# Performance work log

Hardware: AMD Instinct MI355X
Metric: run time of the kernel (lower is better)

The kernel has to match this reference:

```python
import jax, jax.numpy as jnp
import numpy as np
import math

B, S, D, H, L = 16, 1024, 256, 8, 4
OBS, ACT = 160, 96
DH = D // H  # 32, even as required by RoPE
ROPE_BASE = 10000.0
LN_EPS = 1e-5


def setup_inputs() -> dict:
    key = jax.random.key(0)
    ks = jax.random.split(key, 16)
    s = 0.02
    n = jax.random.normal
    return {
        "obs_seq": n(ks[0], (B, S, OBS), jnp.float32),
        "action_seq": n(ks[1], (B, S, ACT), jnp.float32),
        # linears stored as [in, out] (transpose of torch convention)
        "in_W": n(ks[2], (OBS + ACT, D), jnp.float32) * s,
        "in_b": jnp.zeros((D,), jnp.float32),
        "qW": n(ks[3], (L, D, D), jnp.float32) * s,
        "qb": jnp.zeros((L, D), jnp.float32),
        "kW": n(ks[4], (L, D, D), jnp.float32) * s,
        "kb": jnp.zeros((L, D), jnp.float32),
        "vW": n(ks[5], (L, D, D), jnp.float32) * s,
        "vb": jnp.zeros((L, D), jnp.float32),
        "oW": n(ks[6], (L, D, D), jnp.float32) * s,
        "ob": jnp.zeros((L, D), jnp.float32),
        "out_W": n(ks[7], (D, D), jnp.float32) * s,
        "out_b": jnp.zeros((D,), jnp.float32),
        "ln_g": jnp.ones((D,), jnp.float32),
        "ln_b": jnp.zeros((D,), jnp.float32),
    }


def _rope(x):
    # x: [B,H,S,DH]; interleaved real/imag rotation (stride-2 split like torch code)
    pos = jnp.arange(S, dtype=jnp.float32)[:, None]                 # [S,1]
    freq_seq = jnp.arange(0, DH, 2, dtype=jnp.float32)              # [DH/2]
    inv_freq = 1.0 / (ROPE_BASE ** (freq_seq / DH))
    freqs = pos * inv_freq[None, :]                                  # [S,DH/2]
    cos = jnp.cos(freqs)[None, None]                                 # [1,1,S,DH/2]
    sin = jnp.sin(freqs)[None, None]
    xr = x[..., 0::2]
    xi = x[..., 1::2]
    rr = xr * cos - xi * sin
    ri = xr * sin + xi * cos
    # interleave back: [..., DH/2, 2] -> [..., DH]
    return jnp.stack([rr, ri], axis=-1).reshape(x.shape)


def _attn_layer(x, qW, qb, kW, kb, vW, vb, oW, ob):
    def heads(t):
        return t.reshape(B, S, H, DH).transpose(0, 2, 1, 3)  # [B,H,S,DH]
    q = _rope(heads(x @ qW + qb))
    k = _rope(heads(x @ kW + kb))
    v = heads(x @ vW + vb)
    scores = jnp.einsum('bhqd,bhkd->bhqk', q, k) / math.sqrt(DH)
    w = jax.nn.softmax(scores, axis=-1)  # dropout is identity at inference
    o = jnp.einsum('bhqk,bhkd->bhqd', w, v)
    o = o.transpose(0, 2, 1, 3).reshape(B, S, D)
    return o @ oW + ob


def reference(obs_seq, action_seq, in_W, in_b, qW, qb, kW, kb, vW, vb, oW, ob,
              out_W, out_b, ln_g, ln_b):
    x = jnp.concatenate([obs_seq, action_seq], axis=-1) @ in_W + in_b  # [B,S,D]
    for l in range(L):  # residual self-attention stack with RoPE
        x = x + _attn_layer(x, qW[l], qb[l], kW[l], kb[l], vW[l], vb[l], oW[l], ob[l])
    y = x @ out_W + out_b
    mu = jnp.mean(y, axis=-1, keepdims=True)
    var = jnp.mean(jnp.square(y - mu), axis=-1, keepdims=True)
    y = (y - mu) / jnp.sqrt(var + LN_EPS) * ln_g + ln_b
    context_embedding = y[:, -1]       # seq_lengths=None path: last timestep
    sequence_embeddings = y
    return context_embedding, sequence_embeddings
```

## Files before the change

kernel.cpp:

```cpp
#include <hip/hip_runtime.h>
#include <hip/hip_bf16.h>
#include <math.h>

#define B_ 16
#define S_ 1024
#define D_ 256
#define H_ 8
#define L_ 4
#define DH_ 32
#define OBS_ 160
#define ACT_ 96
#define M_ (B_*S_)

typedef __attribute__((ext_vector_type(8)))  short short8v;
typedef __attribute__((ext_vector_type(4)))  short short4v;
typedef __attribute__((ext_vector_type(4)))  float f32x4;
typedef __attribute__((ext_vector_type(4)))  unsigned uint4v;

#define ALPHA_ 0.25507313f

__device__ inline short bf16rne(float x) {
    unsigned u = __builtin_bit_cast(unsigned, x);
    unsigned r = (u + 0x7fffu + ((u >> 16) & 1u)) >> 16;
    return (short)r;
}

#if __has_builtin(__builtin_amdgcn_exp2f)
#define EXP2F(x) __builtin_amdgcn_exp2f(x)
#else
#define EXP2F(x) exp2f(x)
#endif

__device__ inline unsigned cvtpk_bf16(float lo, float hi) {
    unsigned r;
    asm("v_cvt_pk_bf16_f32 %0, %1, %2" : "=v"(r) : "v"(lo), "v"(hi));
    return r;
}

__global__ __launch_bounds__(256) void rope_table_k(float* __restrict__ cosT2,
                                                    float* __restrict__ sinT2) {
    int idx = blockIdx.x * 256 + threadIdx.x;
    int i = idx >> 10, s = idx & 1023;
    float invf = powf(10000.0f, -(float)(2 * i) / 32.0f);
    float ang = (float)s * invf;
    float sn, cs;
    sincosf(ang, &sn, &cs);
    cosT2[idx] = cs;
    sinT2[idx] = sn;
}

__global__ __launch_bounds__(256) void cvt_in_k(const float* __restrict__ obs,
                                                const float* __restrict__ act,
                                                short* __restrict__ xIn) {
    const int idx = (blockIdx.x * 256 + threadIdx.x) * 8;
    const int row = idx >> 8, col = idx & 255;
    const float* s = (col < OBS_) ? (obs + (size_t)row * OBS_ + col)
                                  : (act + (size_t)row * ACT_ + (col - OBS_));
    const float4 v0 = *(const float4*)s;
    const float4 v1 = *(const float4*)(s + 4);
    short8v o = {bf16rne(v0.x), bf16rne(v0.y), bf16rne(v0.z), bf16rne(v0.w),
                 bf16rne(v1.x), bf16rne(v1.y), bf16rne(v1.z), bf16rne(v1.w)};
    *(short8v*)&xIn[idx] = o;
}

__global__ __launch_bounds__(256) void wconv_k(
    const float* __restrict__ qW, const float* __restrict__ kW,
    const float* __restrict__ vW, const float* __restrict__ oW,
    const float* __restrict__ outW, const float* __restrict__ inW,
    short* __restrict__ WTqkv, short* __restrict__ WTo,
    short* __restrict__ WTf, short* __restrict__ WTin)
{
    __shared__ float T[64][65];
    const int z = blockIdx.y;
    const int bx = blockIdx.x;
    const int tr = (bx & 3) * 64, tc = (bx >> 2) * 64;
    const float* src;
    short* dst;
    if (z < 16) {
        int lay = z >> 2, w = z & 3;
        if (w == 0)      { src = qW + lay * 65536; dst = WTqkv + lay * 196608; }
        else if (w == 1) { src = kW + lay * 65536; dst = WTqkv + lay * 196608 + 65536; }
        else if (w == 2) { src = vW + lay * 65536; dst = WTqkv + lay * 196608 + 131072; }
        else             { src = oW + lay * 65536; dst = WTo + lay * 65536; }
    } else if (z == 16) { src = outW; dst = WTf; }
    else                { src = inW;  dst = WTin; }
    const int tid = threadIdx.x;
    #pragma unroll
    for (int it = 0; it < 4; ++it) {
        int r = (tid >> 4) + it * 16, c = (tid & 15) * 4;
        *(float4*)&T[r][c] = *(const float4*)&src[(size_t)(tr + r) * 256 + tc + c];
    }
    __syncthreads();
    #pragma unroll
    for (int it = 0; it < 4; ++it) {
        int n = (tid >> 4) + it * 16, k = (tid & 15) * 4;
        short4v o = {bf16rne(T[k][n]), bf16rne(T[k + 1][n]),
                     bf16rne(T[k + 2][n]), bf16rne(T[k + 3][n])};
        *(short4v*)&dst[(size_t)(tc + n) * 256 + tr + k] = o;
    }
}

template<int EPI>
__global__ __launch_bounds__(256) void gemm_k(
    const short* __restrict__ A, const short* __restrict__ WT,
    const float* __restrict__ bq, const float* __restrict__ bk,
    const float* __restrict__ bv,
    float* __restrict__ xF, short* __restrict__ xB,
    short* __restrict__ Q2, short* __restrict__ K2, short* __restrict__ VT,
    float* __restrict__ yF,
    const float* __restrict__ cosT2, const float* __restrict__ sinT2)
{
    __shared__ short As[2][128 * 32];
    __shared__ short Bs[2][64 * 32];
    const int tid = threadIdx.x;
    const int l = tid & 63;
    const int wid = tid >> 6, wr = wid >> 1, wc = wid & 1;
    const int bn = blockIdx.x * 64, bm = blockIdx.y * 128;

    const short* aSrc0 = A + (size_t)(bm + (tid >> 2)) * 256 + (tid & 3) * 8;
    const short* aSrc1 = aSrc0 + 64 * 256;
    const short* bSrc  = WT + (size_t)(bn + (tid >> 2)) * 256 + (tid & 3) * 8;

    short8v a0 = *(const short8v*)aSrc0;
    short8v a1 = *(const short8v*)aSrc1;
    short8v b0 = *(const short8v*)bSrc;
    *(short8v*)&As[0][tid * 8]         = a0;
    *(short8v*)&As[0][(tid + 256) * 8] = a1;
    *(short8v*)&Bs[0][tid * 8]         = b0;
    __syncthreads();

    f32x4 acc[4][2];
    #pragma unroll
    for (int i = 0; i < 4; ++i)
        #pragma unroll
        for (int j = 0; j < 2; ++j) acc[i][j] = (f32x4){0.f, 0.f, 0.f, 0.f};

    #pragma unroll
    for (int t = 0; t < 8; ++t) {
        const int cur = t & 1;
        short8v na0, na1, nb;
        if (t < 7) {
            const int k = (t + 1) * 32;
            na0 = *(const short8v*)&aSrc0[k];
            na1 = *(const short8v*)&aSrc1[k];
            nb  = *(const short8v*)&bSrc[k];
        }
        short8v af[4], bf[2];
        #pragma unroll
        for (int i = 0; i < 4; ++i)
            af[i] = *(const short8v*)&As[cur][(wr * 64 + i * 16 + (l & 15)) * 32 + (l >> 4) * 8];
        #pragma unroll
        for (int j = 0; j < 2; ++j)
            bf[j] = *(const short8v*)&Bs[cur][(wc * 32 + j * 16 + (l & 15)) * 32 + (l >> 4) * 8];
        #pragma unroll
        for (int i = 0; i < 4; ++i)
            #pragma unroll
            for (int j = 0; j < 2; ++j)
                acc[i][j] = __builtin_amdgcn_mfma_f32_16x16x32_bf16(af[i], bf[j], acc[i][j], 0, 0, 0);
        if (t < 7) {
            const int nxt = cur ^ 1;
            *(short8v*)&As[nxt][tid * 8]         = na0;
            *(short8v*)&As[nxt][(tid + 256) * 8] = na1;
            *(short8v*)&Bs[nxt][tid * 8]         = nb;
            __syncthreads();
        }
    }

    if (EPI == 0) {
        const int region = bn >> 8;
        if (region == 2) {
            #pragma unroll
            for (int i = 0; i < 4; ++i) {
                const int m0 = bm + wr * 64 + i * 16 + ((l >> 4) << 2);
                const int bI = m0 >> 10, s0 = m0 & 1023;
                const int w  = s0 & 31;
                const int sp = (s0 & ~31) | ((((w & 15) >> 2) << 3) | ((w >> 4) << 2));
                #pragma unroll
                for (int j = 0; j < 2; ++j) {
                    const int nl = (bn & 255) + wc * 32 + j * 16 + (l & 15);
                    const float bb = bv[nl];
                    const f32x4 v = acc[i][j];
                    const int h = nl >> 5, dhh = nl & 31;
                    short4v o = {bf16rne(v[0] + bb), bf16rne(v[1] + bb),
                                 bf16rne(v[2] + bb), bf16rne(v[3] + bb)};
                    *(short4v*)&VT[((size_t)((bI * 8 + h) * 32 + dhh) << 10) + sp] = o;
                }
            }
        } else {
            const float* bias = (region == 0) ? bq : bk;
            __syncthreads();
            short* scr = &As[0][0];
            #pragma unroll
            for (int i = 0; i < 4; ++i) {
                const int tl0 = wr * 64 + i * 16 + ((l >> 4) << 2);
                const int s0r = (bm + tl0) & 1023;
                #pragma unroll
                for (int j = 0; j < 2; ++j) {
                    const int ncl = wc * 32 + j * 16 + (l & 15);
                    const int nl = (bn & 255) + ncl;
                    const float bb = bias[nl];
                    f32x4 v = acc[i][j];
                    v[0] += bb; v[1] += bb; v[2] += bb; v[3] += bb;
                    if (region == 0) { v *= ALPHA_; }
                    const int ir = (nl & 31) >> 1;
                    const f32x4 cs = *(const f32x4*)&cosT2[ir * 1024 + s0r];
                    const f32x4 sn = *(const f32x4*)&sinT2[ir * 1024 + s0r];
                    f32x4 pr;
                    #pragma unroll
                    for (int c = 0; c < 4; ++c) pr[c] = __shfl_xor(v[c], 1);
                    const float sg = (nl & 1) ? 1.f : -1.f;
                    #pragma unroll
                    for (int c = 0; c < 4; ++c)
                        v[c] = v[c] * cs[c] + sg * pr[c] * sn[c];
                    #pragma unroll
                    for (int c = 0; c < 4; ++c) {
                        const int tl = tl0 + c;
                        const int pos = (((ncl >> 3) ^ (tl & 7)) << 3) | (ncl & 7);
                        scr[tl * 64 + pos] = bf16rne(v[c]);
                    }
                }
            }
            __syncthreads();
            const int r = tid >> 1, h2 = tid & 1;
            const int tok = bm + r;
            const int bI = tok >> 10, s0 = tok & 1023;
            const int hh = ((bn & 255) >> 5) + h2;
            short* dst = ((region == 0) ? Q2 : K2)
                         + ((size_t)((bI * 8 + hh) * 1024 + s0)) * 32;
            #pragma unroll
            for (int k = 0; k < 4; ++k) {
                const int pos = ((h2 * 4 + k) ^ (r & 7)) << 3;
                *(uint4*)&dst[k * 8] = *(const uint4*)&scr[r * 64 + pos];
            }
        }
    } else {
        #pragma unroll
        for (int i = 0; i < 4; ++i) {
            const int m0 = bm + wr * 64 + i * 16 + ((l >> 4) << 2);
            #pragma unroll
            for (int j = 0; j < 2; ++j) {
                const int nn = bn + wc * 32 + j * 16 + (l & 15);
                const float bb = bq[nn];
                const f32x4 v = acc[i][j];
                #pragma unroll
                for (int c = 0; c < 4; ++c) {
                    float rr = v[c] + bb;
                    const size_t off = (size_t)(m0 + c) * 256 + nn;
                    if (EPI == 1) rr += xF[off];
                    if (EPI == 3) {
                        yF[off] = rr;
                    } else {
                        xF[off] = rr;
                        xB[off] = bf16rne(rr);
                    }
                }
            }
        }
    }
}

__global__ __launch_bounds__(512, 8) void attn_k(
    const short* __restrict__ Q2, const short* __restrict__ K2,
    const short* __restrict__ VT, short* __restrict__ O)
{
    __shared__ short LB[4096];
    const int tid = threadIdx.x;
    const int l = tid & 63, wid = tid >> 6;
    const int head = blockIdx.x & 127;
    const int qt = blockIdx.x >> 7;
    const int q0w = qt * 128 + wid * 16;
    const int lq = l & 15, g = l >> 4;

    const short8v Qf = *(const short8v*)&Q2[((size_t)head * 1024 + q0w + lq) * 32 + g * 8];

    const char* rbase = (const char*)LB + lq * 64 + ((g ^ ((lq >> 1) & 3)) << 4);

    const bool stg = (tid < 256);
    const int  sK  = (tid < 128) ? 1 : 0;
    const int  srow = (tid & 127) >> 2;
    const int  sc   = tid & 3;
    const short* gsrc = nullptr;
    int gstep = 0;
    char* wbase = nullptr;
    if (stg) {
        if (sK) { gsrc = K2 + ((size_t)head * 1024 + srow) * 32 + sc * 8; gstep = 1024; }
        else    { gsrc = VT + ((size_t)head * 32 + srow) * 1024 + sc * 8; gstep = 32; }
        wbase = (char*)LB + (sK ? 0 : 2048) + srow * 64 + ((sc ^ ((srow >> 1) & 3)) << 4);
    }

    f32x4 acc0 = {0.f, 0.f, 0.f, 0.f}, acc1 = {0.f, 0.f, 0.f, 0.f};
    const f32x4 z4 = {0.f, 0.f, 0.f, 0.f};
    float lsum = 0.f;
    short8v r = {};

    if (stg) {
        short8v r0 = *(const short8v*)gsrc; gsrc += gstep;
        r          = *(const short8v*)gsrc; gsrc += gstep;
        *(short8v*)wbase = r0;
    }
    __syncthreads();

#define ATTN_STEP(BUFOFF) do {                                                 \
        short8v Kf0 = *(const short8v*)(rbase + (BUFOFF));                     \
        short8v Kf1 = *(const short8v*)(rbase + (BUFOFF) + 1024);              \
        short8v Vf0 = *(const short8v*)(rbase + (BUFOFF) + 2048);              \
        short8v Vf1 = *(const short8v*)(rbase + (BUFOFF) + 3072);              \
        f32x4 s0 = __builtin_amdgcn_mfma_f32_16x16x32_bf16(Kf0, Qf, z4, 0,0,0);\
        f32x4 s1 = __builtin_amdgcn_mfma_f32_16x16x32_bf16(Kf1, Qf, z4, 0,0,0);\
        float p0 = EXP2F(s0[0]), p1 = EXP2F(s0[1]);                            \
        float p2 = EXP2F(s0[2]), p3 = EXP2F(s0[3]);                            \
        float p4 = EXP2F(s1[0]), p5 = EXP2F(s1[1]);                            \
        float p6 = EXP2F(s1[2]), p7 = EXP2F(s1[3]);                            \
        lsum += ((p0 + p1) + (p2 + p3)) + ((p4 + p5) + (p6 + p7));             \
        uint4v pv = {cvtpk_bf16(p0, p1), cvtpk_bf16(p2, p3),                   \
                     cvtpk_bf16(p4, p5), cvtpk_bf16(p6, p7)};                  \
        short8v Pf = __builtin_bit_cast(short8v, pv);                          \
        acc0 = __builtin_amdgcn_mfma_f32_16x16x32_bf16(Vf0, Pf, acc0, 0,0,0);  \
        acc1 = __builtin_amdgcn_mfma_f32_16x16x32_bf16(Vf1, Pf, acc1, 0,0,0);  \
    } while (0)

    #pragma unroll 1
    for (int i = 0; i < 15; ++i) {
        if (stg) { *(short8v*)(wbase + 4096) = r;
                   r = *(const short8v*)gsrc; gsrc += gstep; }
        ATTN_STEP(0);
        __syncthreads();
        if (stg) { *(short8v*)wbase = r;
                   r = *(const short8v*)gsrc; gsrc += gstep; }
        ATTN_STEP(4096);
        __syncthreads();
    }
    if (stg) { *(short8v*)(wbase + 4096) = r; }
    ATTN_STEP(0);
    __syncthreads();
    ATTN_STEP(4096);
#undef ATTN_STEP

    lsum += __shfl_xor(lsum, 16);
    lsum += __shfl_xor(lsum, 32);
    const float inv = 1.f / lsum;
    const int bI = head >> 3, hh = head & 7;
    short* op = O + ((size_t)(bI * 1024 + q0w + lq)) * 256 + hh * 32 + g * 4;
    short4v o0 = {bf16rne(acc0[0] * inv), bf16rne(acc0[1] * inv),
                  bf16rne(acc0[2] * inv), bf16rne(acc0[3] * inv)};
    short4v o1 = {bf16rne(acc1[0] * inv), bf16rne(acc1[1] * inv),
                  bf16rne(acc1[2] * inv), bf16rne(acc1[3] * inv)};
    *(short4v*)op = o0;
    *(short4v*)(op + 16) = o1;
}

__global__ __launch_bounds__(256) void ln_k(
    const float* __restrict__ y, const float* __restrict__ g,
    const float* __restrict__ bta, float* __restrict__ outp)
{
    const int tid = threadIdx.x;
    const int wave = tid >> 6, lane = tid & 63;
    const int row = blockIdx.x * 4 + wave;
    const int col = lane * 4;
    float4 t = *(const float4*)&y[(size_t)row * 256 + col];
    float sum = t.x + t.y + t.z + t.w;
    float ss  = t.x * t.x + t.y * t.y + t.z * t.z + t.w * t.w;
    #pragma unroll
    for (int off = 32; off; off >>= 1) {
        sum += __shfl_xor(sum, off);
        ss  += __shfl_xor(ss, off);
    }
    float mean = sum * (1.f / 256.f);
    float var  = ss * (1.f / 256.f) - mean * mean;
    float rstd = rsqrtf(var + 1e-5f);
    float4 gv = *(const float4*)&g[col];
    float4 bv = *(const float4*)&bta[col];
    float4 o;
    o.x = (t.x - mean) * rstd * gv.x + bv.x;
    o.y = (t.y - mean) * rstd * gv.y + bv.y;
    o.z = (t.z - mean) * rstd * gv.z + bv.z;
    o.w = (t.w - mean) * rstd * gv.w + bv.w;
    float* seq = outp + B_ * D_;
    *(float4*)&seq[(size_t)row * 256 + col] = o;
    if ((row & (S_ - 1)) == S_ - 1)
        *(float4*)&outp[(size_t)(row >> 10) * 256 + col] = o;
}

extern "C" void kernel_launch(void* const* d_in, const int* in_sizes, int n_in,
                              void* d_out, int out_size, void* d_ws, size_t ws_size,
                              hipStream_t stream)
{
    const float* obs  = (const float*)d_in[0];
    const float* act  = (const float*)d_in[1];
    const float* inW  = (const float*)d_in[2];
    const float* inb  = (const float*)d_in[3];
    const float* qW   = (const float*)d_in[4];
    const float* qb   = (const float*)d_in[5];
    const float* kW   = (const float*)d_in[6];
    const float* kb   = (const float*)d_in[7];
    const float* vW   = (const float*)d_in[8];
    const float* vb   = (const float*)d_in[9];
    const float* oW   = (const float*)d_in[10];
    const float* ob   = (const float*)d_in[11];
    const float* outW = (const float*)d_in[12];
    const float* outb = (const float*)d_in[13];
    const float* lng  = (const float*)d_in[14];
    const float* lnb  = (const float*)d_in[15];
    float* outp = (float*)d_out;

    const size_t MD = (size_t)M_ * D_;
    float* xF    = (float*)d_ws;
    short* xB    = (short*)(xF + MD);
    short* xIn   = xB + MD;
    short* Q2    = xIn + MD;
    short* K2    = Q2 + MD;
    short* VT    = K2 + MD;
    short* Obf   = VT + MD;
    short* WTqkv = Obf + MD;
    short* WTo   = WTqkv + 786432;
    short* WTf   = WTo + 262144;
    short* WTin  = WTf + 65536;
    float* cosT2 = (float*)(WTin + 65536);
    float* sinT2 = cosT2 + 16384;
    float* ybuf  = (float*)Q2;

    rope_table_k<<<64, 256, 0, stream>>>(cosT2, sinT2);
    cvt_in_k<<<2048, 256, 0, stream>>>(obs, act, xIn);
    wconv_k<<<dim3(16, 18), 256, 0, stream>>>(qW, kW, vW, oW, outW, inW,
                                              WTqkv, WTo, WTf, WTin);

    gemm_k<2><<<dim3(4, 128), 256, 0, stream>>>(xIn, WTin, inb, nullptr, nullptr,
            xF, xB, nullptr, nullptr, nullptr, nullptr, nullptr, nullptr);

    for (int lay = 0; lay < L_; ++lay) {
        gemm_k<0><<<dim3(12, 128), 256, 0, stream>>>(xB, WTqkv + lay * 196608,
                qb + lay * 256, kb + lay * 256, vb + lay * 256,
                nullptr, nullptr, Q2, K2, VT, nullptr, cosT2, sinT2);
        attn_k<<<1024, 512, 0, stream>>>(Q2, K2, VT, Obf);
        gemm_k<1><<<dim3(4, 128), 256, 0, stream>>>(Obf, WTo + lay * 65536,
                ob + lay * 256, nullptr, nullptr, xF, xB,
                nullptr, nullptr, nullptr, nullptr, nullptr, nullptr);
    }

    gemm_k<3><<<dim3(4, 128), 256, 0, stream>>>(xB, WTf, outb, nullptr, nullptr,
            nullptr, nullptr, nullptr, nullptr, nullptr, ybuf, nullptr, nullptr);
    ln_k<<<M_ / 4, 256, 0, stream>>>(ybuf, lng, lnb, outp);
}
```

Baseline: 309.2 us.

## Process two 16-query tiles per wave in attention to reuse K/V loads

Each attention wave now handles 32 query rows (two 16-row Q fragments) instead of 16, so every K/V fragment read from shared memory and every staged K/V tile feeds twice as many MFMAs. The grid is halved to 512 blocks and the occupancy hint drops from 8 to 4 blocks per CU to allow for the extra registers. The aim is to cut LDS traffic, global K/V staging and barrier overhead per unit of work. The cost is higher register pressure and fewer blocks to spread across the CUs.

```diff
diff --git a/kernel.cpp b/kernel.cpp
--- a/kernel.cpp
+++ b/kernel.cpp
@@ -259,7 +259,7 @@
     }
 }
 
-__global__ __launch_bounds__(512, 8) void attn_k(
+__global__ __launch_bounds__(512, 4) void attn_k(
     const short* __restrict__ Q2, const short* __restrict__ K2,
     const short* __restrict__ VT, short* __restrict__ O)
 {
@@ -268,10 +268,12 @@
     const int l = tid & 63, wid = tid >> 6;
     const int head = blockIdx.x & 127;
     const int qt = blockIdx.x >> 7;
-    const int q0w = qt * 128 + wid * 16;
+    const int q0w = qt * 256 + wid * 32;
     const int lq = l & 15, g = l >> 4;
 
-    const short8v Qf = *(const short8v*)&Q2[((size_t)head * 1024 + q0w + lq) * 32 + g * 8];
+    const short* qp = &Q2[((size_t)head * 1024 + q0w + lq) * 32 + g * 8];
+    const short8v QfA = *(const short8v*)qp;
+    const short8v QfB = *(const short8v*)(qp + 16 * 32);
 
     const char* rbase = (const char*)LB + lq * 64 + ((g ^ ((lq >> 1) & 3)) << 4);
 
@@ -288,9 +290,10 @@
         wbase = (char*)LB + (sK ? 0 : 2048) + srow * 64 + ((sc ^ ((srow >> 1) & 3)) << 4);
     }
 
-    f32x4 acc0 = {0.f, 0.f, 0.f, 0.f}, acc1 = {0.f, 0.f, 0.f, 0.f};
+    f32x4 aA0 = {0.f,0.f,0.f,0.f}, aA1 = {0.f,0.f,0.f,0.f};
+    f32x4 aB0 = {0.f,0.f,0.f,0.f}, aB1 = {0.f,0.f,0.f,0.f};
     const f32x4 z4 = {0.f, 0.f, 0.f, 0.f};
-    float lsum = 0.f;
+    float lsA = 0.f, lsB = 0.f;
     short8v r = {};
 
     if (stg) {
@@ -305,18 +308,30 @@
         short8v Kf1 = *(const short8v*)(rbase + (BUFOFF) + 1024);              \
         short8v Vf0 = *(const short8v*)(rbase + (BUFOFF) + 2048);              \
         short8v Vf1 = *(const short8v*)(rbase + (BUFOFF) + 3072);              \
-        f32x4 s0 = __builtin_amdgcn_mfma_f32_16x16x32_bf16(Kf0, Qf, z4, 0,0,0);\
-        f32x4 s1 = __builtin_amdgcn_mfma_f32_16x16x32_bf16(Kf1, Qf, z4, 0,0,0);\
-        float p0 = EXP2F(s0[0]), p1 = EXP2F(s0[1]);                            \
-        float p2 = EXP2F(s0[2]), p3 = EXP2F(s0[3]);                            \
-        float p4 = EXP2F(s1[0]), p5 = EXP2F(s1[1]);                            \
-        float p6 = EXP2F(s1[2]), p7 = EXP2F(s1[3]);                            \
-        lsum += ((p0 + p1) + (p2 + p3)) + ((p4 + p5) + (p6 + p7));             \
-        uint4v pv = {cvtpk_bf16(p0, p1), cvtpk_bf16(p2, p3),                   \
-                     cvtpk_bf16(p4, p5), cvtpk_bf16(p6, p7)};                  \
-        short8v Pf = __builtin_bit_cast(short8v, pv);                          \
-        acc0 = __builtin_amdgcn_mfma_f32_16x16x32_bf16(Vf0, Pf, acc0, 0,0,0);  \
-        acc1 = __builtin_amdgcn_mfma_f32_16x16x32_bf16(Vf1, Pf, acc1, 0,0,0);  \
+        f32x4 sA0 = __builtin_amdgcn_mfma_f32_16x16x32_bf16(Kf0, QfA, z4, 0,0,0);\
+        f32x4 sA1 = __builtin_amdgcn_mfma_f32_16x16x32_bf16(Kf1, QfA, z4, 0,0,0);\
+        f32x4 sB0 = __builtin_amdgcn_mfma_f32_16x16x32_bf16(Kf0, QfB, z4, 0,0,0);\
+        f32x4 sB1 = __builtin_amdgcn_mfma_f32_16x16x32_bf16(Kf1, QfB, z4, 0,0,0);\
+        float pa0 = EXP2F(sA0[0]), pa1 = EXP2F(sA0[1]);                        \
+        float pa2 = EXP2F(sA0[2]), pa3 = EXP2F(sA0[3]);                        \
+        float pa4 = EXP2F(sA1[0]), pa5 = EXP2F(sA1[1]);                        \
+        float pa6 = EXP2F(sA1[2]), pa7 = EXP2F(sA1[3]);                        \
+        lsA += ((pa0 + pa1) + (pa2 + pa3)) + ((pa4 + pa5) + (pa6 + pa7));      \
+        uint4v pva = {cvtpk_bf16(pa0, pa1), cvtpk_bf16(pa2, pa3),              \
+                      cvtpk_bf16(pa4, pa5), cvtpk_bf16(pa6, pa7)};             \
+        short8v PfA = __builtin_bit_cast(short8v, pva);                        \
+        aA0 = __builtin_amdgcn_mfma_f32_16x16x32_bf16(Vf0, PfA, aA0, 0,0,0);   \
+        aA1 = __builtin_amdgcn_mfma_f32_16x16x32_bf16(Vf1, PfA, aA1, 0,0,0);   \
+        float pb0 = EXP2F(sB0[0]), pb1 = EXP2F(sB0[1]);                        \
+        float pb2 = EXP2F(sB0[2]), pb3 = EXP2F(sB0[3]);                        \
+        float pb4 = EXP2F(sB1[0]), pb5 = EXP2F(sB1[1]);                        \
+        float pb6 = EXP2F(sB1[2]), pb7 = EXP2F(sB1[3]);                        \
+        lsB += ((pb0 + pb1) + (pb2 + pb3)) + ((pb4 + pb5) + (pb6 + pb7));      \
+        uint4v pvb = {cvtpk_bf16(pb0, pb1), cvtpk_bf16(pb2, pb3),              \
+                      cvtpk_bf16(pb4, pb5), cvtpk_bf16(pb6, pb7)};             \
+        short8v PfB = __builtin_bit_cast(short8v, pvb);                        \
+        aB0 = __builtin_amdgcn_mfma_f32_16x16x32_bf16(Vf0, PfB, aB0, 0,0,0);   \
+        aB1 = __builtin_amdgcn_mfma_f32_16x16x32_bf16(Vf1, PfB, aB1, 0,0,0);   \
     } while (0)
 
     #pragma unroll 1
@@ -336,17 +351,27 @@
     ATTN_STEP(4096);
 #undef ATTN_STEP
 
-    lsum += __shfl_xor(lsum, 16);
-    lsum += __shfl_xor(lsum, 32);
-    const float inv = 1.f / lsum;
+    lsA += __shfl_xor(lsA, 16);
+    lsA += __shfl_xor(lsA, 32);
+    lsB += __shfl_xor(lsB, 16);
+    lsB += __shfl_xor(lsB, 32);
+    const float invA = 1.f / lsA;
+    const float invB = 1.f / lsB;
     const int bI = head >> 3, hh = head & 7;
     short* op = O + ((size_t)(bI * 1024 + q0w + lq)) * 256 + hh * 32 + g * 4;
-    short4v o0 = {bf16rne(acc0[0] * inv), bf16rne(acc0[1] * inv),
-                  bf16rne(acc0[2] * inv), bf16rne(acc0[3] * inv)};
-    short4v o1 = {bf16rne(acc1[0] * inv), bf16rne(acc1[1] * inv),
-                  bf16rne(acc1[2] * inv), bf16rne(acc1[3] * inv)};
-    *(short4v*)op = o0;
-    *(short4v*)(op + 16) = o1;
+    short4v oA0 = {bf16rne(aA0[0] * invA), bf16rne(aA0[1] * invA),
+                   bf16rne(aA0[2] * invA), bf16rne(aA0[3] * invA)};
+    short4v oA1 = {bf16rne(aA1[0] * invA), bf16rne(aA1[1] * invA),
+                   bf16rne(aA1[2] * invA), bf16rne(aA1[3] * invA)};
+    *(short4v*)op = oA0;
+    *(short4v*)(op + 16) = oA1;
+    short* opB = op + 16 * 256;
+    short4v oB0 = {bf16rne(aB0[0] * invB), bf16rne(aB0[1] * invB),
+                   bf16rne(aB0[2] * invB), bf16rne(aB0[3] * invB)};
+    short4v oB1 = {bf16rne(aB1[0] * invB), bf16rne(aB1[1] * invB),
+                   bf16rne(aB1[2] * invB), bf16rne(aB1[3] * invB)};
+    *(short4v*)opB = oB0;
+    *(short4v*)(opB + 16) = oB1;
 }
 
 __global__ __launch_bounds__(256) void ln_k(
@@ -431,7 +456,7 @@
         gemm_k<0><<<dim3(12, 128), 256, 0, stream>>>(xB, WTqkv + lay * 196608,
                 qb + lay * 256, kb + lay * 256, vb + lay * 256,
                 nullptr, nullptr, Q2, K2, VT, nullptr, cosT2, sinT2);
-        attn_k<<<1024, 512, 0, stream>>>(Q2, K2, VT, Obf);
+        attn_k<<<512, 512, 0, stream>>>(Q2, K2, VT, Obf);
         gemm_k<1><<<dim3(4, 128), 256, 0, stream>>>(Obf, WTo + lay * 65536,
                 ob + lay * 256, nullptr, nullptr, xF, xB,
                 nullptr, nullptr, nullptr, nullptr, nullptr, nullptr);
```

Measured after the change: 308.4 us. No clear change (-0.2%).

## Stage whole per-head K/V in LDS and process 64 queries per wave

Applied to the files above, without the earlier changes.

The attention kernel now copies the full K and V for one head (128 KB) into shared memory once. It then loops over all keys with no barriers, and each wave handles four 16-query fragments that reuse every K/V fragment read from shared memory. The grid drops from 1024 to 256 blocks and the launch bound allows only two blocks per CU. This removes the double-buffered per-step staging and its per-step __syncthreads. In exchange, occupancy falls to roughly one block per CU, and the up-front global-to-LDS load can no longer overlap with compute.

```diff
diff --git a/kernel.cpp b/kernel.cpp
--- a/kernel.cpp
+++ b/kernel.cpp
@@ -259,94 +259,99 @@
     }
 }
 
-__global__ __launch_bounds__(512, 8) void attn_k(
+__global__ __launch_bounds__(512, 2) void attn_k(
     const short* __restrict__ Q2, const short* __restrict__ K2,
     const short* __restrict__ VT, short* __restrict__ O)
 {
-    __shared__ short LB[4096];
+    __shared__ short lb[65536];
     const int tid = threadIdx.x;
     const int l = tid & 63, wid = tid >> 6;
     const int head = blockIdx.x & 127;
-    const int qt = blockIdx.x >> 7;
-    const int q0w = qt * 128 + wid * 16;
+    const int qh = blockIdx.x >> 7;
+    const int q0w = qh * 512 + wid * 64;
     const int lq = l & 15, g = l >> 4;
 
-    const short8v Qf = *(const short8v*)&Q2[((size_t)head * 1024 + q0w + lq) * 32 + g * 8];
-
-    const char* rbase = (const char*)LB + lq * 64 + ((g ^ ((lq >> 1) & 3)) << 4);
-
-    const bool stg = (tid < 256);
-    const int  sK  = (tid < 128) ? 1 : 0;
-    const int  srow = (tid & 127) >> 2;
-    const int  sc   = tid & 3;
-    const short* gsrc = nullptr;
-    int gstep = 0;
-    char* wbase = nullptr;
-    if (stg) {
-        if (sK) { gsrc = K2 + ((size_t)head * 1024 + srow) * 32 + sc * 8; gstep = 1024; }
-        else    { gsrc = VT + ((size_t)head * 32 + srow) * 1024 + sc * 8; gstep = 32; }
-        wbase = (char*)LB + (sK ? 0 : 2048) + srow * 64 + ((sc ^ ((srow >> 1) & 3)) << 4);
-    }
-
-    f32x4 acc0 = {0.f, 0.f, 0.f, 0.f}, acc1 = {0.f, 0.f, 0.f, 0.f};
+    const short* Kh = K2 + (size_t)head * 32768;
+    const short* Vh = VT + (size_t)head * 32768;
+
+    #pragma unroll
+    for (int i = 0; i < 8; ++i) {
+        const int c = tid + i * 512;
+        short8v kv = *(const short8v*)(Kh + c * 8);
+        const int key = c >> 2, dc = c & 3;
+        *(short8v*)((char*)lb + key * 64 + ((dc ^ ((key >> 1) & 3)) << 4)) = kv;
+        short8v vv = *(const short8v*)(Vh + c * 8);
+        const int dh = c >> 7, kc = c & 127;
+        *(short8v*)((char*)lb + 65536 + (kc >> 2) * 2048 + dh * 64
+                    + (((kc & 3) ^ ((dh >> 1) & 3)) << 4)) = vv;
+    }
+
+    const short* qp = Q2 + ((size_t)head * 1024 + q0w + lq) * 32 + g * 8;
+    const short8v QfA = *(const short8v*)qp;
+    const short8v QfB = *(const short8v*)(qp + 512);
+    const short8v QfC = *(const short8v*)(qp + 1024);
+    const short8v QfD = *(const short8v*)(qp + 1536);
+
+    const char* LBK = (const char*)lb + lq * 64 + ((g ^ ((lq >> 1) & 3)) << 4);
+    const char* LBV = LBK + 65536;
+
+    f32x4 aA0 = {0.f,0.f,0.f,0.f}, aA1 = {0.f,0.f,0.f,0.f};
+    f32x4 aB0 = {0.f,0.f,0.f,0.f}, aB1 = {0.f,0.f,0.f,0.f};
+    f32x4 aC0 = {0.f,0.f,0.f,0.f}, aC1 = {0.f,0.f,0.f,0.f};
+    f32x4 aD0 = {0.f,0.f,0.f,0.f}, aD1 = {0.f,0.f,0.f,0.f};
     const f32x4 z4 = {0.f, 0.f, 0.f, 0.f};
-    float lsum = 0.f;
-    short8v r = {};
-
-    if (stg) {
-        short8v r0 = *(const short8v*)gsrc; gsrc += gstep;
-        r          = *(const short8v*)gsrc; gsrc += gstep;
-        *(short8v*)wbase = r0;
-    }
+    float lsA = 0.f, lsB = 0.f, lsC = 0.f, lsD = 0.f;
+
     __syncthreads();
 
-#define ATTN_STEP(BUFOFF) do {                                                 \
-        short8v Kf0 = *(const short8v*)(rbase + (BUFOFF));                     \
-        short8v Kf1 = *(const short8v*)(rbase + (BUFOFF) + 1024);              \
-        short8v Vf0 = *(const short8v*)(rbase + (BUFOFF) + 2048);              \
-        short8v Vf1 = *(const short8v*)(rbase + (BUFOFF) + 3072);              \
-        f32x4 s0 = __builtin_amdgcn_mfma_f32_16x16x32_bf16(Kf0, Qf, z4, 0,0,0);\
-        f32x4 s1 = __builtin_amdgcn_mfma_f32_16x16x32_bf16(Kf1, Qf, z4, 0,0,0);\
+#define QSTEP(QF, A0, A1, LS) do {                                             \
+        f32x4 s0 = __builtin_amdgcn_mfma_f32_16x16x32_bf16(Kf0, QF, z4, 0,0,0);\
+        f32x4 s1 = __builtin_amdgcn_mfma_f32_16x16x32_bf16(Kf1, QF, z4, 0,0,0);\
         float p0 = EXP2F(s0[0]), p1 = EXP2F(s0[1]);                            \
         float p2 = EXP2F(s0[2]), p3 = EXP2F(s0[3]);                            \
         float p4 = EXP2F(s1[0]), p5 = EXP2F(s1[1]);                            \
         float p6 = EXP2F(s1[2]), p7 = EXP2F(s1[3]);                            \
-        lsum += ((p0 + p1) + (p2 + p3)) + ((p4 + p5) + (p6 + p7));             \
+        LS += ((p0 + p1) + (p2 + p3)) + ((p4 + p5) + (p6 + p7));               \
         uint4v pv = {cvtpk_bf16(p0, p1), cvtpk_bf16(p2, p3),                   \
                      cvtpk_bf16(p4, p5), cvtpk_bf16(p6, p7)};                  \
         short8v Pf = __builtin_bit_cast(short8v, pv);                          \
-        acc0 = __builtin_amdgcn_mfma_f32_16x16x32_bf16(Vf0, Pf, acc0, 0,0,0);  \
-        acc1 = __builtin_amdgcn_mfma_f32_16x16x32_bf16(Vf1, Pf, acc1, 0,0,0);  \
+        A0 = __builtin_amdgcn_mfma_f32_16x16x32_bf16(Vf0, Pf, A0, 0,0,0);      \
+        A1 = __builtin_amdgcn_mfma_f32_16x16x32_bf16(Vf1, Pf, A1, 0,0,0);      \
     } while (0)
 
-    #pragma unroll 1
-    for (int i = 0; i < 15; ++i) {
-        if (stg) { *(short8v*)(wbase + 4096) = r;
-                   r = *(const short8v*)gsrc; gsrc += gstep; }
-        ATTN_STEP(0);
-        __syncthreads();
-        if (stg) { *(short8v*)wbase = r;
-                   r = *(const short8v*)gsrc; gsrc += gstep; }
-        ATTN_STEP(4096);
-        __syncthreads();
-    }
-    if (stg) { *(short8v*)(wbase + 4096) = r; }
-    ATTN_STEP(0);
-    __syncthreads();
-    ATTN_STEP(4096);
-#undef ATTN_STEP
-
-    lsum += __shfl_xor(lsum, 16);
-    lsum += __shfl_xor(lsum, 32);
-    const float inv = 1.f / lsum;
+    #pragma unroll 4
+    for (int t = 0; t < 32; ++t) {
+        const short8v Kf0 = *(const short8v*)(LBK + t * 2048);
+        const short8v Kf1 = *(const short8v*)(LBK + t * 2048 + 1024);
+        const short8v Vf0 = *(const short8v*)(LBV + t * 2048);
+        const short8v Vf1 = *(const short8v*)(LBV + t * 2048 + 1024);
+        QSTEP(QfA, aA0, aA1, lsA);
+        QSTEP(QfB, aB0, aB1, lsB);
+        QSTEP(QfC, aC0, aC1, lsC);
+        QSTEP(QfD, aD0, aD1, lsD);
+    }
+#undef QSTEP
+
+    lsA += __shfl_xor(lsA, 16); lsA += __shfl_xor(lsA, 32);
+    lsB += __shfl_xor(lsB, 16); lsB += __shfl_xor(lsB, 32);
+    lsC += __shfl_xor(lsC, 16); lsC += __shfl_xor(lsC, 32);
+    lsD += __shfl_xor(lsD, 16); lsD += __shfl_xor(lsD, 32);
     const int bI = head >> 3, hh = head & 7;
     short* op = O + ((size_t)(bI * 1024 + q0w + lq)) * 256 + hh * 32 + g * 4;
-    short4v o0 = {bf16rne(acc0[0] * inv), bf16rne(acc0[1] * inv),
-                  bf16rne(acc0[2] * inv), bf16rne(acc0[3] * inv)};
-    short4v o1 = {bf16rne(acc1[0] * inv), bf16rne(acc1[1] * inv),
-                  bf16rne(acc1[2] * inv), bf16rne(acc1[3] * inv)};
-    *(short4v*)op = o0;
-    *(short4v*)(op + 16) = o1;
+#define QOUT(A0, A1, LS, ROFF) do {                                            \
+        const float inv = 1.f / (LS);                                          \
+        short4v o0 = {bf16rne(A0[0] * inv), bf16rne(A0[1] * inv),              \
+                      bf16rne(A0[2] * inv), bf16rne(A0[3] * inv)};             \
+        short4v o1 = {bf16rne(A1[0] * inv), bf16rne(A1[1] * inv),              \
+                      bf16rne(A1[2] * inv), bf16rne(A1[3] * inv)};             \
+        *(short4v*)(op + (ROFF) * 256) = o0;                                   \
+        *(short4v*)(op + (ROFF) * 256 + 16) = o1;                              \
+    } while (0)
+    QOUT(aA0, aA1, lsA, 0);
+    QOUT(aB0, aB1, lsB, 16);
+    QOUT(aC0, aC1, lsC, 32);
+    QOUT(aD0, aD1, lsD, 48);
+#undef QOUT
 }
 
 __global__ __launch_bounds__(256) void ln_k(
@@ -431,7 +436,7 @@
         gemm_k<0><<<dim3(12, 128), 256, 0, stream>>>(xB, WTqkv + lay * 196608,
                 qb + lay * 256, kb + lay * 256, vb + lay * 256,
                 nullptr, nullptr, Q2, K2, VT, nullptr, cosT2, sinT2);
-        attn_k<<<1024, 512, 0, stream>>>(Q2, K2, VT, Obf);
+        attn_k<<<256, 512, 0, stream>>>(Q2, K2, VT, Obf);
         gemm_k<1><<<dim3(4, 128), 256, 0, stream>>>(Obf, WTo + lay * 65536,
                 ob + lay * 256, nullptr, nullptr, xF, xB,
                 nullptr, nullptr, nullptr, nullptr, nullptr, nullptr);
```

New measurement: 309.2 us. About the same (-0.0%).
